# Performance work log

Hardware: AMD Instinct MI355X
Metric: run time of the kernel (lower is better)

Reference implementation:

```python
import jax, jax.numpy as jnp
import numpy as np

N_NODES = 100000
N_EDGES = 1600000   # avg in-degree 16
D_IN = 128
D_HID = 256
N_CLASSES = 40
N_GRAPHS = 64


def setup_inputs() -> dict:
    key = jax.random.key(0)
    ks = jax.random.split(key, 8)
    h = jax.random.normal(ks[0], (N_NODES, D_IN), dtype=jnp.float32)
    src = jax.random.randint(ks[1], (N_EDGES,), 0, N_NODES, dtype=jnp.int64)
    dst = jax.random.randint(ks[2], (N_EDGES,), 0, N_NODES, dtype=jnp.int64)
    graph_ids = jnp.sort(jax.random.randint(ks[3], (N_NODES,), 0, N_GRAPHS, dtype=jnp.int64))
    s_in = 1.0 / np.sqrt(D_IN)
    s_hid = 1.0 / np.sqrt(D_HID)
    W_self = jax.random.uniform(ks[4], (D_IN, D_HID), jnp.float32, -s_in, s_in)
    W_neigh = jax.random.uniform(ks[5], (D_IN, D_HID), jnp.float32, -s_in, s_in)
    b = jnp.zeros((D_HID,), jnp.float32)
    W_pred = jax.random.uniform(ks[6], (D_HID, N_CLASSES), jnp.float32, -s_hid, s_hid)
    b_pred = jnp.zeros((N_CLASSES,), jnp.float32)
    return {"h": h, "W_self": W_self, "W_neigh": W_neigh, "b": b,
            "W_pred": W_pred, "b_pred": b_pred,
            "src": src, "dst": dst, "graph_ids": graph_ids}


def reference(h, W_self, W_neigh, b, W_pred, b_pred, src, dst, graph_ids):
    n_nodes = h.shape[0]
    # --- SAGEConv 'mean': mean over in-neighbors (gather src feats, scatter-add to dst) ---
    deg = jax.ops.segment_sum(jnp.ones_like(dst, dtype=h.dtype), dst, num_segments=n_nodes)
    agg = jax.ops.segment_sum(h[src], dst, num_segments=n_nodes)  # [N, D_IN]
    h_neigh = agg / jnp.maximum(deg, 1.0)[:, None]  # zero-in-degree -> 0
    hid = jax.nn.relu(h @ W_self + h_neigh @ W_neigh + b)  # [N, D_HID]
    # --- AvgPooling per graph ---
    cnt = jax.ops.segment_sum(jnp.ones((n_nodes,), h.dtype), graph_ids, num_segments=N_GRAPHS)
    pooled = jax.ops.segment_sum(hid, graph_ids, num_segments=N_GRAPHS) / jnp.maximum(cnt, 1.0)[:, None]
    # --- prediction head (dropout is identity in eval) ---
    return pooled @ W_pred + b_pred  # [N_GRAPHS, N_CLASSES]
```

## Files before the change

### kernel.cpp

```cpp
#include <hip/hip_runtime.h>
#include <stdint.h>

constexpr int kNodes    = 100000;
constexpr int kEdges    = 1600000;
constexpr int kDin      = 128;
constexpr int kK        = 256;
constexpr int kDhid     = 256;
constexpr int kClasses  = 40;
constexpr int kGraphs   = 64;

constexpr int kBktShift = 8;
constexpr int NB = (kNodes + 255) >> 8;
constexpr int kBktCap = 5120;
constexpr int kChunk = 3125;
constexpr int kEBlocks = kEdges / kChunk;
constexpr int kSCT = 1024;
constexpr int kCvtBlocks = (kNodes * 32 + kK * kDhid) / kSCT;

constexpr int kTPB = 5;
constexpr int kTiles = kNodes / 32;
constexpr int kGemmBlocks = kTiles / kTPB;

typedef __attribute__((ext_vector_type(8))) short bf8_t;
typedef __attribute__((ext_vector_type(4))) float f4_t;
typedef __attribute__((ext_vector_type(2))) float f2_t;

__device__ inline ushort f2bf(float f) {
  uint32_t u = __float_as_uint(f);
  u += 0x7fff + ((u >> 16) & 1);
  return (ushort)(u >> 16);
}

template <bool HI>
__device__ inline f2_t fp8x2_f32(uint32_t w) {
#if __has_builtin(__builtin_amdgcn_cvt_pk_f32_fp8)
  return __builtin_amdgcn_cvt_pk_f32_fp8(w, HI);
#else
  f2_t r;
  uint32_t b0 = HI ? ((w >> 16) & 0xffu) : (w & 0xffu);
  uint32_t b1 = HI ? (w >> 24) : ((w >> 8) & 0xffu);
  auto dec = [](uint32_t b) -> float {
    uint32_t s = (b & 0x80u) << 24;
    uint32_t em = b & 0x7fu;
    float mag;
    if (em >= 0x08u) {
      uint32_t e = (em >> 3) - 7 + 127;
      mag = __uint_as_float((e << 23) | ((em & 7u) << 20));
    } else {
      mag = (float)em * 0.001953125f;
    }
    return __uint_as_float(s | __float_as_uint(mag));
  };
  r.x = dec(b0); r.y = dec(b1);
  return r;
#endif
}

__device__ inline uint32_t f32_to_e4m3(float f) {
  uint32_t sgn = (__float_as_uint(f) >> 31) << 7;
  float mag = fabsf(f);
  uint32_t r;
  if (mag >= 0.015625f) {
    uint32_t u = __float_as_uint(mag);
    u += 0x7FFFF + ((u >> 20) & 1);
    int e = (int)(u >> 23) - 127;
    if (e > 8) r = 0x7Eu;
    else r = (uint32_t)((e + 7) << 3) | ((u >> 20) & 7u);
  } else {
    float m = mag * 512.f;
    int mi = (int)rintf(m);
    r = (mi > 7) ? 0x08u : (uint32_t)mi;
  }
  return r | sgn;
}

__device__ inline uint32_t pack4_e4m3(float x, float y, float z, float w) {
#if __has_builtin(__builtin_amdgcn_cvt_pk_fp8_f32)
  uint32_t p = __builtin_amdgcn_cvt_pk_fp8_f32(x, y, 0u, false);
  return __builtin_amdgcn_cvt_pk_fp8_f32(z, w, p, true);
#else
  return f32_to_e4m3(x) | (f32_to_e4m3(y) << 8) |
         (f32_to_e4m3(z) << 16) | (f32_to_e4m3(w) << 24);
#endif
}

__global__ void zero_ws(float* __restrict__ gsum, int* __restrict__ bktCur) {
  int t = blockIdx.x * 256 + threadIdx.x;
  if (t < kGraphs * kDhid) gsum[t] = 0.f;
  int u = t - kGraphs * kDhid;
  if (u >= 0 && u < NB) bktCur[u] = 0;
}

__global__ __launch_bounds__(kSCT)
void scatter_cvt(const int* __restrict__ src, const int* __restrict__ dst,
                 int* __restrict__ bktCur, uint32_t* __restrict__ pairs,
                 const float* __restrict__ h, const float* __restrict__ Ws,
                 const float* __restrict__ Wn, ushort* __restrict__ A16,
                 ushort* __restrict__ Wt, uint8_t* __restrict__ H8,
                 int scatterBlocks) {
  __shared__ int hist[NB], base[NB], cur[NB];
  if ((int)blockIdx.x < scatterBlocks) {
    for (int i = threadIdx.x; i < NB; i += kSCT) { hist[i] = 0; cur[i] = 0; }
    __syncthreads();
    int e0 = blockIdx.x * kChunk;
    int e1 = min(e0 + kChunk, kEdges);
    for (int e = e0 + threadIdx.x; e < e1; e += kSCT)
      atomicAdd(&hist[dst[e] >> kBktShift], 1);
    __syncthreads();
    for (int i = threadIdx.x; i < NB; i += kSCT)
      base[i] = hist[i] ? atomicAdd(&bktCur[i], hist[i]) : 0;
    __syncthreads();
    for (int e = e0 + threadIdx.x; e < e1; e += kSCT) {
      int d = dst[e];
      int b = d >> kBktShift;
      int p = atomicAdd(&cur[b], 1);
      pairs[(size_t)b * kBktCap + base[b] + p] = ((uint32_t)src[e] << 8) | (uint32_t)(d & 255);
    }
  } else {
    int t = ((int)blockIdx.x - scatterBlocks) * kSCT + threadIdx.x;
    const int hN = kNodes * 32;
    if (t < hN) {
      int n = t >> 5;
      int c4 = (t & 31) * 4;
      float4 v = *reinterpret_cast<const float4*>(h + (size_t)n * kDin + c4);
      ushort4 o;
      o.x = f2bf(v.x); o.y = f2bf(v.y); o.z = f2bf(v.z); o.w = f2bf(v.w);
      *reinterpret_cast<ushort4*>(A16 + (size_t)n * kK + c4) = o;
      *reinterpret_cast<uint32_t*>(H8 + (size_t)n * kDin + c4) =
          pack4_e4m3(v.x, v.y, v.z, v.w);
    } else {
      int u = t - hN;
      int j = u & 255;
      int k = u >> 8;
      float v = (k < 128) ? Ws[(size_t)k * kDhid + j] : Wn[(size_t)(k - 128) * kDhid + j];
      Wt[(size_t)j * kK + k] = f2bf(v);
    }
  }
}

__global__ void bucket_fill(const uint32_t* __restrict__ pairs, const int* __restrict__ bktCur,
                            int* __restrict__ row, int* __restrict__ rend,
                            int* __restrict__ csr) {
  __shared__ int deg[256], scn[256], cur[256];
  int b = blockIdx.x;
  int t = threadIdx.x;
  int cnt = bktCur[b];
  int e0 = b * kBktCap;
  int nb0 = b << kBktShift;
  deg[t] = 0;
  __syncthreads();
  for (int e = t; e < cnt; e += 256)
    atomicAdd(&deg[pairs[e0 + e] & 255u], 1);
  __syncthreads();
  int d = deg[t];
  scn[t] = d;
  __syncthreads();
#pragma unroll
  for (int off = 1; off < 256; off <<= 1) {
    int u = (t >= off) ? scn[t - off] : 0;
    __syncthreads();
    scn[t] += u;
    __syncthreads();
  }
  int excl = scn[t] - d;
  cur[t] = excl;
  int n = nb0 + t;
  if (n < kNodes) { row[n] = e0 + excl; rend[n] = e0 + scn[t]; }
  __syncthreads();
  for (int e = t; e < cnt; e += 256) {
    uint32_t pr = pairs[e0 + e];
    int p = atomicAdd(&cur[pr & 255u], 1);
    csr[e0 + p] = (int)(pr >> 8);
  }
}

__global__ void aggregate8(const uint8_t* __restrict__ H8, ushort* __restrict__ A16,
                           const int* __restrict__ row, const int* __restrict__ rend,
                           const int* __restrict__ csr) {
  int wv = (blockIdx.x * 256 + threadIdx.x) >> 6;
  int lane = threadIdx.x & 63;
  int grp = lane >> 4;
  int sub = lane & 15;
  int n = wv * 4 + grp;
  int s0 = row[n], s1 = rend[n];
  float a0 = 0.f, a1 = 0.f, a2 = 0.f, a3 = 0.f, a4 = 0.f, a5 = 0.f, a6 = 0.f, a7 = 0.f;
#pragma unroll 4
  for (int i = s0; i < s1; ++i) {
    int s = csr[i];
    uint2 v = *reinterpret_cast<const uint2*>(H8 + (size_t)s * kDin + sub * 8);
    f2_t l0 = fp8x2_f32<false>(v.x), h0 = fp8x2_f32<true>(v.x);
    f2_t l1 = fp8x2_f32<false>(v.y), h1 = fp8x2_f32<true>(v.y);
    a0 += l0.x; a1 += l0.y; a2 += h0.x; a3 += h0.y;
    a4 += l1.x; a5 += l1.y; a6 += h1.x; a7 += h1.y;
  }
  float rd = 1.f / fmaxf((float)(s1 - s0), 1.f);
  uint4 o;
  o.x = (uint32_t)f2bf(a0 * rd) | ((uint32_t)f2bf(a1 * rd) << 16);
  o.y = (uint32_t)f2bf(a2 * rd) | ((uint32_t)f2bf(a3 * rd) << 16);
  o.z = (uint32_t)f2bf(a4 * rd) | ((uint32_t)f2bf(a5 * rd) << 16);
  o.w = (uint32_t)f2bf(a6 * rd) | ((uint32_t)f2bf(a7 * rd) << 16);
  *reinterpret_cast<uint4*>((char*)A16 + (size_t)n * 512 + 256 + sub * 16) = o;
}

__global__ __launch_bounds__(256, 2)
void gemm_pool(const ushort* __restrict__ A16, const ushort* __restrict__ Wt,
               const float* __restrict__ bias, const int* __restrict__ gid,
               float* __restrict__ gsum) {
  __shared__ ushort Abuf[2][32 * 256];
  const int tid  = threadIdx.x;
  const int lane = tid & 63;
  const int wave = tid >> 6;
  const int lhi = lane >> 4;
  const int llo = lane & 15;

  bf8_t bfr[4][8];
#pragma unroll
  for (int nf = 0; nf < 4; ++nf) {
    const char* wrow = (const char*)Wt + (size_t)(wave * 64 + nf * 16 + llo) * 512 + lhi * 16;
#pragma unroll
    for (int kk = 0; kk < 8; ++kk)
      bfr[nf][kk] = *reinterpret_cast<const bf8_t*>(wrow + kk * 64);
  }
  float bv[4];
#pragma unroll
  for (int nf = 0; nf < 4; ++nf) bv[nf] = bias[wave * 64 + nf * 16 + llo];

  auto stage = [&](int buf, int tile) {
#pragma unroll
    for (int i = 0; i < 4; ++i) {
      int r = i * 8 + (tid >> 5);
      int wb = (tid & 31) * 16;
      size_t gsrc = ((size_t)tile * 32 + r) * 512 + (size_t)(wb ^ ((r & 7) << 4));
      uint32_t ldst = (uint32_t)(i * 4096 + tid * 16);
      __builtin_amdgcn_global_load_lds(
          (const __attribute__((address_space(1))) uint32_t*)((const char*)A16 + gsrc),
          (__attribute__((address_space(3))) uint32_t*)((char*)&Abuf[buf][0] + ldst),
          16, 0, 0);
    }
  };

  const int t0 = blockIdx.x * kTPB;
  stage(0, t0);

  float pooled[4] = {0.f, 0.f, 0.f, 0.f};
  int cur_g = gid[t0 * 32];

  for (int ti = 0; ti < kTPB; ++ti) {
    int tile = t0 + ti;
    if (ti + 1 < kTPB) {
      stage((ti + 1) & 1, tile + 1);
      asm volatile("s_waitcnt vmcnt(4)" ::: "memory");
    } else {
      asm volatile("s_waitcnt vmcnt(0)" ::: "memory");
    }
    __builtin_amdgcn_s_barrier();
    __builtin_amdgcn_sched_barrier(0);

    f4_t acc[2][4];
#pragma unroll
    for (int mf = 0; mf < 2; ++mf)
#pragma unroll
      for (int nf = 0; nf < 4; ++nf) acc[mf][nf] = (f4_t)0.f;
    const char* abase = (const char*)&Abuf[ti & 1][0];
    const int swz = (llo & 7) << 4;
#pragma unroll
    for (int kk = 0; kk < 8; ++kk) {
      int kb = kk * 64 + lhi * 16;
      bf8_t x0 = *reinterpret_cast<const bf8_t*>(abase + llo * 512 + (kb ^ swz));
      bf8_t x1 = *reinterpret_cast<const bf8_t*>(abase + (16 + llo) * 512 + (kb ^ swz));
#pragma unroll
      for (int nf = 0; nf < 4; ++nf) {
        acc[0][nf] = __builtin_amdgcn_mfma_f32_16x16x32_bf16(x0, bfr[nf][kk], acc[0][nf], 0, 0, 0);
        acc[1][nf] = __builtin_amdgcn_mfma_f32_16x16x32_bf16(x1, bfr[nf][kk], acc[1][nf], 0, 0, 0);
      }
    }

    int base = tile * 32;
    int gA = gid[base], gB = gid[base + 31];
    if (gA == gB) {
      if (gA != cur_g) {
#pragma unroll
        for (int nf = 0; nf < 4; ++nf) {
          if (pooled[nf] != 0.f)
            atomicAdd(&gsum[cur_g * kDhid + wave * 64 + nf * 16 + llo], pooled[nf]);
          pooled[nf] = 0.f;
        }
        cur_g = gA;
      }
#pragma unroll
      for (int nf = 0; nf < 4; ++nf) {
        float s = 0.f;
#pragma unroll
        for (int mf = 0; mf < 2; ++mf)
#pragma unroll
          for (int q = 0; q < 4; ++q) s += fmaxf(acc[mf][nf][q] + bv[nf], 0.f);
        pooled[nf] += s;
      }
    } else {
#pragma unroll
      for (int mf = 0; mf < 2; ++mf)
#pragma unroll
        for (int q = 0; q < 4; ++q) {
          int r = base + mf * 16 + lhi * 4 + q;
          int g = gid[r];
#pragma unroll
          for (int nf = 0; nf < 4; ++nf) {
            float v = fmaxf(acc[mf][nf][q] + bv[nf], 0.f);
            if (v != 0.f) atomicAdd(&gsum[g * kDhid + wave * 64 + nf * 16 + llo], v);
          }
        }
    }
    __builtin_amdgcn_sched_barrier(0);
    __builtin_amdgcn_s_barrier();
  }

#pragma unroll
  for (int nf = 0; nf < 4; ++nf)
    if (pooled[nf] != 0.f)
      atomicAdd(&gsum[cur_g * kDhid + wave * 64 + nf * 16 + llo], pooled[nf]);
}

__global__ void head_kernel(const float* __restrict__ gsum,
                            const float* __restrict__ Wp,
                            const float* __restrict__ bp,
                            const int* __restrict__ gid,
                            float* __restrict__ out) {
  int g = blockIdx.x;
  int c = threadIdx.x;
  int lo0 = 0, hi0 = kNodes;
  while (lo0 < hi0) { int m = (lo0 + hi0) >> 1; if (gid[m] < g) lo0 = m + 1; else hi0 = m; }
  int lo1 = lo0, hi1 = kNodes;
  while (lo1 < hi1) { int m = (lo1 + hi1) >> 1; if (gid[m] < g + 1) lo1 = m + 1; else hi1 = m; }
  float rc = 1.0f / fmaxf((float)(lo1 - lo0), 1.0f);
  if (c < kClasses) {
    float acc = bp[c];
    for (int k = 0; k < kDhid; ++k)
      acc += gsum[g * kDhid + k] * rc * Wp[k * kClasses + c];
    out[g * kClasses + c] = acc;
  }
}

extern "C" void kernel_launch(void* const* d_in, const int* in_sizes, int n_in,
                              void* d_out, int out_size, void* d_ws, size_t ws_size,
                              hipStream_t stream) {
  const float* h  = (const float*)d_in[0];
  const float* Ws = (const float*)d_in[1];
  const float* Wn = (const float*)d_in[2];
  const float* b  = (const float*)d_in[3];
  const float* Wp = (const float*)d_in[4];
  const float* bp = (const float*)d_in[5];
  const int* src  = (const int*)d_in[6];
  const int* dst  = (const int*)d_in[7];
  const int* gid  = (const int*)d_in[8];
  float* out = (float*)d_out;

  char* ws = (char*)d_ws;
  const size_t a16Off    = 0;
  const size_t wtOff     = 51249152;
  const size_t csrOff    = 51380224;
  const size_t rowOff    = 59408384;
  const size_t rendOff   = 59808384;
  const size_t gsumOff   = 60208384;
  const size_t bktCurOff = 60273920;
  const size_t h8Off     = 60275712;
  const size_t pairsOff  = 73075712;
  const size_t needBig   = pairsOff + 8028160;
  ushort* A16     = (ushort*)(ws + a16Off);
  ushort* Wt      = (ushort*)(ws + wtOff);
  int* csr        = (int*)(ws + csrOff);
  int* row        = (int*)(ws + rowOff);
  int* rend       = (int*)(ws + rendOff);
  float* gsum     = (float*)(ws + gsumOff);
  int* bktCur     = (int*)(ws + bktCurOff);
  uint8_t* H8     = (uint8_t*)(ws + h8Off);
  const bool bigWs = (ws_size >= needBig);
  uint32_t* pairs = bigWs ? (uint32_t*)(ws + pairsOff) : (uint32_t*)(ws + a16Off);

  {
    int nz = kGraphs * kDhid + NB;
    hipLaunchKernelGGL(zero_ws, dim3((nz + 255) / 256), dim3(256), 0, stream, gsum, bktCur);
  }

  if (bigWs) {
    hipLaunchKernelGGL(scatter_cvt, dim3(kEBlocks + kCvtBlocks), dim3(kSCT), 0, stream,
                       src, dst, bktCur, pairs, h, Ws, Wn, A16, Wt, H8, kEBlocks);
    hipLaunchKernelGGL(bucket_fill, dim3(NB), dim3(256), 0, stream,
                       pairs, bktCur, row, rend, csr);
  } else {
    hipLaunchKernelGGL(scatter_cvt, dim3(kEBlocks), dim3(kSCT), 0, stream,
                       src, dst, bktCur, pairs, h, Ws, Wn, A16, Wt, H8, kEBlocks);
    hipLaunchKernelGGL(bucket_fill, dim3(NB), dim3(256), 0, stream,
                       pairs, bktCur, row, rend, csr);
    hipLaunchKernelGGL(scatter_cvt, dim3(kCvtBlocks), dim3(kSCT), 0, stream,
                       src, dst, bktCur, pairs, h, Ws, Wn, A16, Wt, H8, 0);
  }

  hipLaunchKernelGGL(aggregate8, dim3(kNodes / 16), dim3(256), 0, stream,
                     H8, A16, row, rend, csr);

  hipLaunchKernelGGL(gemm_pool, dim3(kGemmBlocks), dim3(256), 0, stream,
                     A16, Wt, b, gid, gsum);
  hipLaunchKernelGGL(head_kernel, dim3(kGraphs), dim3(64), 0, stream,
                     gsum, Wp, bp, gid, out);
}
```

Measured before the change: 144.5 us.

## Replicate pooled-sum buffers and reduce atomics with wave shuffles

The pooled per-graph sums now go to 8 replicated buffers, picked by block index and placed in the pairs workspace after the bucket step has used it. This spreads atomic contention on the 64x256 graph sums. Partial pools are reduced across the lane groups with shuffles before the atomic, so fewer atomics are issued. The head kernel sums the replicas into shared memory. The edge chunk per scatter block is doubled, halving the number of scatter blocks. The cost is an extra zero launch between aggregation and GEMM, plus a small amount of extra head work.

```diff
diff --git a/kernel.cpp b/kernel.cpp
--- a/kernel.cpp
+++ b/kernel.cpp
@@ -12,7 +12,7 @@
 constexpr int kBktShift = 8;
 constexpr int NB = (kNodes + 255) >> 8;
 constexpr int kBktCap = 5120;
-constexpr int kChunk = 3125;
+constexpr int kChunk = 6250;
 constexpr int kEBlocks = kEdges / kChunk;
 constexpr int kSCT = 1024;
 constexpr int kCvtBlocks = (kNodes * 32 + kK * kDhid) / kSCT;
@@ -20,6 +20,7 @@
 constexpr int kTPB = 5;
 constexpr int kTiles = kNodes / 32;
 constexpr int kGemmBlocks = kTiles / kTPB;
+constexpr int kRepl = 8;
 
 typedef __attribute__((ext_vector_type(8))) short bf8_t;
 typedef __attribute__((ext_vector_type(4))) float f4_t;
@@ -84,11 +85,14 @@
 #endif
 }
 
-__global__ void zero_ws(float* __restrict__ gsum, int* __restrict__ bktCur) {
+__global__ void zero_bkt(int* __restrict__ bktCur) {
   int t = blockIdx.x * 256 + threadIdx.x;
-  if (t < kGraphs * kDhid) gsum[t] = 0.f;
-  int u = t - kGraphs * kDhid;
-  if (u >= 0 && u < NB) bktCur[u] = 0;
+  if (t < NB) bktCur[t] = 0;
+}
+
+__global__ void zero_gsum(float* __restrict__ g, int n) {
+  int t = blockIdx.x * 256 + threadIdx.x;
+  if (t < n) g[t] = 0.f;
 }
 
 __global__ __launch_bounds__(kSCT)
@@ -205,13 +209,14 @@
 __global__ __launch_bounds__(256, 2)
 void gemm_pool(const ushort* __restrict__ A16, const ushort* __restrict__ Wt,
                const float* __restrict__ bias, const int* __restrict__ gid,
-               float* __restrict__ gsum) {
+               float* __restrict__ gsumR, int replMask) {
   __shared__ ushort Abuf[2][32 * 256];
   const int tid  = threadIdx.x;
   const int lane = tid & 63;
   const int wave = tid >> 6;
   const int lhi = lane >> 4;
   const int llo = lane & 15;
+  float* gout = gsumR + (size_t)(blockIdx.x & replMask) * (kGraphs * kDhid);
 
   bf8_t bfr[4][8];
 #pragma unroll
@@ -245,6 +250,18 @@
   float pooled[4] = {0.f, 0.f, 0.f, 0.f};
   int cur_g = gid[t0 * 32];
 
+  auto flushp = [&](int g) {
+#pragma unroll
+    for (int nf = 0; nf < 4; ++nf) {
+      float v = pooled[nf];
+      v += __shfl_xor(v, 16, 64);
+      v += __shfl_xor(v, 32, 64);
+      if (lhi == 0 && v != 0.f)
+        atomicAdd(&gout[g * kDhid + wave * 64 + nf * 16 + llo], v);
+      pooled[nf] = 0.f;
+    }
+  };
+
   for (int ti = 0; ti < kTPB; ++ti) {
     int tile = t0 + ti;
     if (ti + 1 < kTPB) {
@@ -278,15 +295,7 @@
     int base = tile * 32;
     int gA = gid[base], gB = gid[base + 31];
     if (gA == gB) {
-      if (gA != cur_g) {
-#pragma unroll
-        for (int nf = 0; nf < 4; ++nf) {
-          if (pooled[nf] != 0.f)
-            atomicAdd(&gsum[cur_g * kDhid + wave * 64 + nf * 16 + llo], pooled[nf]);
-          pooled[nf] = 0.f;
-        }
-        cur_g = gA;
-      }
+      if (gA != cur_g) { flushp(cur_g); cur_g = gA; }
 #pragma unroll
       for (int nf = 0; nf < 4; ++nf) {
         float s = 0.f;
@@ -306,37 +315,39 @@
 #pragma unroll
           for (int nf = 0; nf < 4; ++nf) {
             float v = fmaxf(acc[mf][nf][q] + bv[nf], 0.f);
-            if (v != 0.f) atomicAdd(&gsum[g * kDhid + wave * 64 + nf * 16 + llo], v);
+            if (v != 0.f) atomicAdd(&gout[g * kDhid + wave * 64 + nf * 16 + llo], v);
           }
         }
     }
     __builtin_amdgcn_sched_barrier(0);
     __builtin_amdgcn_s_barrier();
   }
-
-#pragma unroll
-  for (int nf = 0; nf < 4; ++nf)
-    if (pooled[nf] != 0.f)
-      atomicAdd(&gsum[cur_g * kDhid + wave * 64 + nf * 16 + llo], pooled[nf]);
-}
-
-__global__ void head_kernel(const float* __restrict__ gsum,
+  flushp(cur_g);
+}
+
+__global__ void head_kernel(const float* __restrict__ gsumR, int nrepl,
                             const float* __restrict__ Wp,
                             const float* __restrict__ bp,
                             const int* __restrict__ gid,
                             float* __restrict__ out) {
+  __shared__ float sgs[kDhid];
   int g = blockIdx.x;
-  int c = threadIdx.x;
+  int t = threadIdx.x;
   int lo0 = 0, hi0 = kNodes;
   while (lo0 < hi0) { int m = (lo0 + hi0) >> 1; if (gid[m] < g) lo0 = m + 1; else hi0 = m; }
   int lo1 = lo0, hi1 = kNodes;
   while (lo1 < hi1) { int m = (lo1 + hi1) >> 1; if (gid[m] < g + 1) lo1 = m + 1; else hi1 = m; }
   float rc = 1.0f / fmaxf((float)(lo1 - lo0), 1.0f);
-  if (c < kClasses) {
-    float acc = bp[c];
+  float s = 0.f;
+  for (int r = 0; r < nrepl; ++r)
+    s += gsumR[(size_t)r * (kGraphs * kDhid) + g * kDhid + t];
+  sgs[t] = s * rc;
+  __syncthreads();
+  if (t < kClasses) {
+    float acc = bp[t];
     for (int k = 0; k < kDhid; ++k)
-      acc += gsum[g * kDhid + k] * rc * Wp[k * kClasses + c];
-    out[g * kClasses + c] = acc;
+      acc += sgs[k] * Wp[k * kClasses + t];
+    out[g * kClasses + t] = acc;
   }
 }
 
@@ -370,16 +381,14 @@
   int* csr        = (int*)(ws + csrOff);
   int* row        = (int*)(ws + rowOff);
   int* rend       = (int*)(ws + rendOff);
-  float* gsum     = (float*)(ws + gsumOff);
   int* bktCur     = (int*)(ws + bktCurOff);
   uint8_t* H8     = (uint8_t*)(ws + h8Off);
   const bool bigWs = (ws_size >= needBig);
   uint32_t* pairs = bigWs ? (uint32_t*)(ws + pairsOff) : (uint32_t*)(ws + a16Off);
-
-  {
-    int nz = kGraphs * kDhid + NB;
-    hipLaunchKernelGGL(zero_ws, dim3((nz + 255) / 256), dim3(256), 0, stream, gsum, bktCur);
-  }
+  const int nrepl = bigWs ? kRepl : 1;
+  float* gsumR    = bigWs ? (float*)(ws + pairsOff) : (float*)(ws + gsumOff);
+
+  hipLaunchKernelGGL(zero_bkt, dim3((NB + 255) / 256), dim3(256), 0, stream, bktCur);
 
   if (bigWs) {
     hipLaunchKernelGGL(scatter_cvt, dim3(kEBlocks + kCvtBlocks), dim3(kSCT), 0, stream,
@@ -398,8 +407,13 @@
   hipLaunchKernelGGL(aggregate8, dim3(kNodes / 16), dim3(256), 0, stream,
                      H8, A16, row, rend, csr);
 
+  {
+    int n = nrepl * kGraphs * kDhid;
+    hipLaunchKernelGGL(zero_gsum, dim3((n + 255) / 256), dim3(256), 0, stream, gsumR, n);
+  }
+
   hipLaunchKernelGGL(gemm_pool, dim3(kGemmBlocks), dim3(256), 0, stream,
-                     A16, Wt, b, gid, gsum);
-  hipLaunchKernelGGL(head_kernel, dim3(kGraphs), dim3(64), 0, stream,
-                     gsum, Wp, bp, gid, out);
-}
+                     A16, Wt, b, gid, gsumR, nrepl - 1);
+  hipLaunchKernelGGL(head_kernel, dim3(kGraphs), dim3(kDhid), 0, stream,
+                     gsumR, nrepl, Wp, bp, gid, out);
+}
```

Result: faster. 132.9 us (-8.0%).
